# Optimization experiments

Hardware: AMD Instinct MI355X
Metric: run time of the kernel (lower is better)

The kernel has to match this reference:

```python
import jax, jax.numpy as jnp
import numpy as np

B, N, D = 8, 1024, 768
H = 12
HD = D // H


def setup_inputs() -> dict:
    key = jax.random.key(0)
    ks = jax.random.split(key, 9)
    s = 1.0 / np.sqrt(D)
    return {
        "x": jax.random.normal(ks[0], (B, N, D), dtype=jnp.float32),
        "Wq": jax.random.normal(ks[1], (D, D), dtype=jnp.float32) * s,
        "bq": jax.random.normal(ks[2], (D,), dtype=jnp.float32) * 0.02,
        "Wk": jax.random.normal(ks[3], (D, D), dtype=jnp.float32) * s,
        "bk": jax.random.normal(ks[4], (D,), dtype=jnp.float32) * 0.02,
        "Wv": jax.random.normal(ks[5], (D, D), dtype=jnp.float32) * s,
        "bv": jax.random.normal(ks[6], (D,), dtype=jnp.float32) * 0.02,
        "Wo": jax.random.normal(ks[7], (D, D), dtype=jnp.float32) * s,
        "bo": jax.random.normal(ks[8], (D,), dtype=jnp.float32) * 0.02,
    }


def _softmax_one(x):
    # quiet softmax: exp(x - max) / (1 + sum exp(x - max))
    x = x - jnp.max(x, axis=-1, keepdims=True)
    ex = jnp.exp(x)
    return ex / (1.0 + jnp.sum(ex, axis=-1, keepdims=True))


def reference(x, Wq, bq, Wk, bk, Wv, bv, Wo, bo):
    q = x @ Wq + bq  # [B,N,D]
    k = x @ Wk + bk
    v = x @ Wv + bv
    # split heads -> [B,H,N,HD]
    qs = q.reshape(B, N, H, HD).transpose(0, 2, 1, 3)
    ks = k.reshape(B, N, H, HD).transpose(0, 2, 1, 3)
    vs = v.reshape(B, N, H, HD).transpose(0, 2, 1, 3)
    scores = jnp.einsum("bhqd,bhkd->bhqk", qs, ks) / np.sqrt(HD)
    attn = _softmax_one(scores)  # quiet_attention=True
    ctx = jnp.einsum("bhqk,bhkd->bhqd", attn, vs)
    ctx = ctx.transpose(0, 2, 1, 3).reshape(B, N, D)
    return ctx @ Wo + bo
```

## Files before the change

kernel.cpp:

```cpp
#include <hip/hip_runtime.h>
#include <cstdint>

#define DEV __device__ __forceinline__

typedef __bf16 bf16x4 __attribute__((ext_vector_type(4)));
typedef __bf16 bf16x8 __attribute__((ext_vector_type(8)));
typedef float  floatx4 __attribute__((ext_vector_type(4)));
typedef short  short4v __attribute__((ext_vector_type(4)));

constexpr int BB = 8, NSEQ = 1024, DMODEL = 768, NH = 12, HD = 64;
constexpr int MTOK = BB * NSEQ;
constexpr int NQKV = 3 * DMODEL;
constexpr float CS = 0.18033688011112042f;

DEV void async_copy16(void* lds, const void* g) {
    __builtin_amdgcn_global_load_lds(
        (__attribute__((address_space(1))) void*)(const_cast<void*>(g)),
        (__attribute__((address_space(3))) void*)lds,
        16, 0, 0);
}

DEV floatx4 mfma16x32(bf16x8 a, bf16x8 b, floatx4 c) {
    return __builtin_amdgcn_mfma_f32_16x16x32_bf16(a, b, c, 0, 0, 0);
}
DEV floatx4 mfma16x16(bf16x4 a, bf16x4 b, floatx4 c) {
    return __builtin_amdgcn_mfma_f32_16x16x16bf16_1k(
        __builtin_bit_cast(short4v, a), __builtin_bit_cast(short4v, b), c, 0, 0, 0);
}


__global__ __launch_bounds__(256) void k_prep(const float* __restrict__ x,
                                              __bf16* __restrict__ xb,
                                              const float* __restrict__ Wq,
                                              const float* __restrict__ Wk,
                                              const float* __restrict__ Wv,
                                              const float* __restrict__ Wo,
                                              __bf16* __restrict__ wtqkv,
                                              __bf16* __restrict__ wto,
                                              const float* __restrict__ bq,
                                              const float* __restrict__ bk,
                                              const float* __restrict__ bv,
                                              float* __restrict__ bqkv) {
    __shared__ float tile[32][33];
    int bid = blockIdx.x, t = threadIdx.x;
    if (bid < 6144) {
        int i = (bid * 256 + t) * 4;
        float4 v = *(const float4*)(x + i);
        bf16x4 o;
        o[0] = (__bf16)v.x; o[1] = (__bf16)v.y; o[2] = (__bf16)v.z; o[3] = (__bf16)v.w;
        *(bf16x4*)(xb + i) = o;
    } else if (bid < 8448) {
        int idx = bid - 6144;
        int z = idx / 576, rem = idx % 576;
        int k0 = (rem % 24) * 32, n0 = (rem / 24) * 32;
        const float* W = (z == 0) ? Wq : (z == 1) ? Wk : (z == 2) ? Wv : Wo;
        int tx = t & 31, ty = t >> 5;
#pragma unroll
        for (int p = 0; p < 4; p++)
            tile[ty + 8 * p][tx] = W[(size_t)(k0 + ty + 8 * p) * 768 + n0 + tx];
        __syncthreads();
        __bf16* out = (z < 3) ? (wtqkv + (size_t)z * 768 * 768) : wto;
#pragma unroll
        for (int p = 0; p < 4; p++)
            out[(size_t)(n0 + ty + 8 * p) * 768 + k0 + tx] = (__bf16)tile[tx][ty + 8 * p];
    } else {
        int i = (bid - 8448) * 256 + t;
        if (i < 768) bqkv[i] = bq[i];
        else if (i < 1536) bqkv[i] = bk[i - 768];
        else bqkv[i] = bv[i - 1536];
    }
}

template <typename OutT, bool QKV, int BN>
__global__ __launch_bounds__(256) void k_gemm(const __bf16* __restrict__ A,
                                              const __bf16* __restrict__ Bt,
                                              const float* __restrict__ bias,
                                              OutT* __restrict__ C, int Nn,
                                              __bf16* __restrict__ qfb,
                                              __bf16* __restrict__ kfb,
                                              __bf16* __restrict__ vfb) {
    constexpr int CT = BN / 32;
    constexpr int NBI = BN / 32;
    __shared__ __align__(16) __bf16 As[128 * 64];
    __shared__ __align__(16) __bf16 Bs[BN * 64];
    int t = threadIdx.x, lane = t & 63, w = t >> 6;
    int quad = lane >> 4, n16 = lane & 15;
    int wm = w & 1, wn = w >> 1;
    int m0 = blockIdx.x * 128, n0 = blockIdx.y * BN;
    floatx4 acc[4][CT] = {};

    for (int k0 = 0; k0 < 768; k0 += 64) {
        __syncthreads();
#pragma unroll
        for (int i = 0; i < 4; i++) {
            int off = t + i * 256;
            int row = off >> 3, pc = off & 7;
            int c = pc ^ (row & 7);
            async_copy16(&As[row * 64 + pc * 8],
                         &A[(size_t)(m0 + row) * 768 + k0 + c * 8]);
        }
#pragma unroll
        for (int i = 0; i < NBI; i++) {
            int off = t + i * 256;
            int row = off >> 3, pc = off & 7;
            int c = pc ^ (row & 7);
            async_copy16(&Bs[row * 64 + pc * 8],
                         &Bt[(size_t)(n0 + row) * 768 + k0 + c * 8]);
        }
        __builtin_amdgcn_s_waitcnt(0);
        __syncthreads();
#pragma unroll
        for (int kfi = 0; kfi < 2; kfi++) {
            bf16x8 a[4], bfr[CT];
#pragma unroll
            for (int rt = 0; rt < 4; rt++) {
                int row = wm * 64 + rt * 16 + n16;
                a[rt] = *(const bf16x8*)&As[row * 64 + ((quad + 4 * kfi) ^ (row & 7)) * 8];
            }
#pragma unroll
            for (int ct = 0; ct < CT; ct++) {
                int row = wn * (BN / 2) + ct * 16 + n16;
                bfr[ct] = *(const bf16x8*)&Bs[row * 64 + ((quad + 4 * kfi) ^ (row & 7)) * 8];
            }
#pragma unroll
            for (int rt = 0; rt < 4; rt++)
#pragma unroll
                for (int ct = 0; ct < CT; ct++)
                    acc[rt][ct] = mfma16x32(a[rt], bfr[ct], acc[rt][ct]);
        }
    }

    if (QKV) {
        if (n0 >= 1536) {
#pragma unroll
            for (int ct = 0; ct < CT; ct++) {
                int col = n0 + wn * (BN / 2) + ct * 16 + n16;
                float bs = bias[col];
                int cz = col - 1536;
                int hh = cz >> 6, hd = cz & 63;
                int mg = hd >> 4, l16 = hd & 15;
#pragma unroll
                for (int rt = 0; rt < 4; rt++) {
                    int row0 = m0 + wm * 64 + rt * 16 + quad * 4;
                    int bb = row0 >> 10, key = row0 & 1023;
                    int kt = key >> 6, wv = (key >> 4) & 3, qd = (key >> 2) & 3;
                    bf16x4 pk;
#pragma unroll
                    for (int r = 0; r < 4; r++) pk[r] = (__bf16)(acc[rt][ct][r] + bs);
                    size_t idx = ((((size_t)(bb * 12 + hh) * 16 + kt) * 4 + wv) * 4 + mg) * 256
                                 + (size_t)(qd * 16 + l16) * 4;
                    *(bf16x4*)&vfb[idx] = pk;
                }
            }
        } else {
            __bf16* dst = (n0 < 768) ? qfb : kfb;
            float mult = (n0 < 768) ? CS : 1.0f;
            int cofs = (n0 < 768) ? 0 : 768;
#pragma unroll
            for (int ct = 0; ct < CT; ct++) {
                int col = n0 + wn * (BN / 2) + ct * 16 + n16;
                float bs = bias[col];
                int cz = col - cofs;
                int hh = cz >> 6, hd = cz & 63;
                int kfi = hd >> 5, qd2 = (hd >> 3) & 3, j = hd & 7;
#pragma unroll
                for (int rt = 0; rt < 4; rt++) {
                    int row0 = m0 + wm * 64 + rt * 16 + quad * 4;
                    int bb = row0 >> 10, q = row0 & 1023;
                    int t16 = q >> 4, nn = q & 15;
                    size_t idx = (((size_t)(bb * 12 + hh) * 64 + t16) * 2 + kfi) * 512
                                 + (size_t)(qd2 * 16 + nn) * 8 + j;
#pragma unroll
                    for (int r = 0; r < 4; r++)
                        dst[idx + (size_t)r * 8] = (__bf16)((acc[rt][ct][r] + bs) * mult);
                }
            }
        }
    } else {
#pragma unroll
        for (int ct = 0; ct < CT; ct++) {
            int col = n0 + wn * (BN / 2) + ct * 16 + n16;
            float bs = bias[col];
#pragma unroll
            for (int rt = 0; rt < 4; rt++) {
#pragma unroll
                for (int r = 0; r < 4; r++) {
                    int row = m0 + wm * 64 + rt * 16 + quad * 4 + r;
                    C[(size_t)row * Nn + col] = (OutT)(acc[rt][ct][r] + bs);
                }
            }
        }
    }
}

__global__ __launch_bounds__(256) void k_attn(const __bf16* __restrict__ QF,
                                              const __bf16* __restrict__ KF,
                                              const __bf16* __restrict__ VF,
                                              __bf16* __restrict__ ctx) {
    __shared__ __align__(16) unsigned char smem[18432];
    float* buf0 = (float*)smem;
    float* buf1 = (float*)(smem + 8704);
    float* Lsum = (float*)(smem + 17408);
    float* Pmax = (float*)(smem + 17920);

    int t = threadIdx.x, lane = t & 63, w = t >> 6;
    int quad = lane >> 4, n16 = lane & 15;
    int id = blockIdx.x;
    int bB = id & 7;
    int seq = id >> 3;
    int h = seq % 12;
    int qt = seq / 12;
    int q0 = qt * 32;
    int bh = bB * NH + h;

    bf16x8 qf[2][2];
    {
        const __bf16* qp = QF + (size_t)(bh * 64 + qt * 2) * 1024 + lane * 8;
#pragma unroll
        for (int ng = 0; ng < 2; ng++)
#pragma unroll
            for (int kfi = 0; kfi < 2; kfi++)
                qf[ng][kfi] = *(const bf16x8*)(qp + (ng * 2 + kfi) * 512);
    }
    const __bf16* kp = KF + (size_t)(bh * 64 + w) * 1024 + lane * 8;
    const __bf16* vp = VF + ((size_t)bh * 16 * 4 + w) * 1024 + lane * 4;

    floatx4 acc[4][2] = {};
    float rs[2] = {0.f, 0.f};
    float pm[2] = {0.f, 0.f};

    auto compute = [&](bf16x8 (&kf)[2], bf16x4 (&vf)[4]) {
        floatx4 s[2] = {};
#pragma unroll
        for (int ng = 0; ng < 2; ng++)
#pragma unroll
            for (int kfi = 0; kfi < 2; kfi++)
                s[ng] = mfma16x32(kf[kfi], qf[ng][kfi], s[ng]);
        bf16x4 pb[2];
#pragma unroll
        for (int ng = 0; ng < 2; ng++) {
#pragma unroll
            for (int r = 0; r < 4; r++) {
                float p = __builtin_amdgcn_exp2f(s[ng][r]);
                rs[ng] += p;
                pm[ng] = fmaxf(pm[ng], p);
                pb[ng][r] = (__bf16)p;
            }
        }
#pragma unroll
        for (int mg = 0; mg < 4; mg++)
#pragma unroll
            for (int ng = 0; ng < 2; ng++)
                acc[mg][ng] = mfma16x16(vf[mg], pb[ng], acc[mg][ng]);
    };

    bf16x8 kf0[2], kf1[2];
    bf16x4 vf0[4], vf1[4];
    kf0[0] = *(const bf16x8*)kp;
    kf0[1] = *(const bf16x8*)(kp + 512);
#pragma unroll
    for (int mg = 0; mg < 4; mg++) vf0[mg] = *(const bf16x4*)(vp + mg * 256);
    kp += 4096; vp += 4096;

    for (int kt = 0; kt < 16; kt += 2) {
        kf1[0] = *(const bf16x8*)kp;
        kf1[1] = *(const bf16x8*)(kp + 512);
#pragma unroll
        for (int mg = 0; mg < 4; mg++) vf1[mg] = *(const bf16x4*)(vp + mg * 256);
        kp += 4096; vp += 4096;
        compute(kf0, vf0);
        if (kt < 14) {
            kf0[0] = *(const bf16x8*)kp;
            kf0[1] = *(const bf16x8*)(kp + 512);
#pragma unroll
            for (int mg = 0; mg < 4; mg++) vf0[mg] = *(const bf16x4*)(vp + mg * 256);
            kp += 4096; vp += 4096;
        }
        compute(kf1, vf1);
    }

#pragma unroll
    for (int ng = 0; ng < 2; ng++) {
        rs[ng] += __shfl_xor(rs[ng], 16);
        rs[ng] += __shfl_xor(rs[ng], 32);
        pm[ng] = fmaxf(pm[ng], __shfl_xor(pm[ng], 16));
        pm[ng] = fmaxf(pm[ng], __shfl_xor(pm[ng], 32));
    }
    if (quad < 2) {
        Lsum[w * 32 + quad * 16 + n16] = quad ? rs[1] : rs[0];
        Pmax[w * 32 + quad * 16 + n16] = quad ? pm[1] : pm[0];
    }
    __syncthreads();

    float* mybuf = (w & 1) ? buf1 : buf0;
    if (w < 2) {
#pragma unroll
        for (int mg = 0; mg < 4; mg++)
#pragma unroll
            for (int ng = 0; ng < 2; ng++)
                *(floatx4*)&mybuf[(ng * 16 + n16) * 68 + mg * 16 + quad * 4] = acc[mg][ng];
    }
    __syncthreads();
    if (w >= 2) {
#pragma unroll
        for (int mg = 0; mg < 4; mg++)
#pragma unroll
            for (int ng = 0; ng < 2; ng++) {
                float* p = &mybuf[(ng * 16 + n16) * 68 + mg * 16 + quad * 4];
                floatx4 cur = *(const floatx4*)p;
                *(floatx4*)p = cur + acc[mg][ng];
            }
    }
    __syncthreads();

    int qrow = t >> 3;
    int hh = (t & 7) * 8;
    float l = Lsum[qrow] + Lsum[32 + qrow] + Lsum[64 + qrow] + Lsum[96 + qrow];
    float pmx = fmaxf(fmaxf(Pmax[qrow], Pmax[32 + qrow]),
                      fmaxf(Pmax[64 + qrow], Pmax[96 + qrow]));
    float invd = 1.f / (pmx + l);
    floatx4 v0 = *(const floatx4*)&buf0[qrow * 68 + hh];
    floatx4 v1 = *(const floatx4*)&buf0[qrow * 68 + hh + 4];
    floatx4 u0 = *(const floatx4*)&buf1[qrow * 68 + hh];
    floatx4 u1 = *(const floatx4*)&buf1[qrow * 68 + hh + 4];
    bf16x8 o;
#pragma unroll
    for (int j = 0; j < 4; j++) o[j] = (__bf16)((v0[j] + u0[j]) * invd);
#pragma unroll
    for (int j = 0; j < 4; j++) o[j + 4] = (__bf16)((v1[j] + u1[j]) * invd);
    __bf16* dst = ctx + (size_t)(bB * NSEQ + q0 + qrow) * DMODEL + h * 64 + hh;
    *(bf16x8*)dst = o;
}

extern "C" void kernel_launch(void* const* d_in, const int* in_sizes, int n_in,
                              void* d_out, int out_size, void* d_ws, size_t ws_size,
                              hipStream_t stream) {
    (void)in_sizes; (void)n_in; (void)out_size;
    const float* x  = (const float*)d_in[0];
    const float* Wq = (const float*)d_in[1];
    const float* bq = (const float*)d_in[2];
    const float* Wk = (const float*)d_in[3];
    const float* bk = (const float*)d_in[4];
    const float* Wv = (const float*)d_in[5];
    const float* bv = (const float*)d_in[6];
    const float* Wo = (const float*)d_in[7];
    const float* bo = (const float*)d_in[8];
    float* out = (float*)d_out;

    char* ws = (char*)d_ws;
    size_t off = 0;
    auto alloc = [&](size_t bytes) {
        void* p = ws + off;
        off += (bytes + 255) & ~(size_t)255;
        return p;
    };
    __bf16* xb    = (__bf16*)alloc((size_t)MTOK * DMODEL * 2);
    __bf16* wtqkv = (__bf16*)alloc((size_t)NQKV * DMODEL * 2);
    __bf16* wto   = (__bf16*)alloc((size_t)DMODEL * DMODEL * 2);
    float*  bqkv  = (float*)alloc((size_t)NQKV * 4);
    __bf16* qfb   = (__bf16*)alloc((size_t)MTOK * DMODEL * 2);
    __bf16* kfb   = (__bf16*)alloc((size_t)MTOK * DMODEL * 2);
    __bf16* vfb   = (__bf16*)alloc((size_t)MTOK * DMODEL * 2);
    if (off > ws_size) return;
    __bf16* ctx = xb;

    k_prep<<<dim3(8457), dim3(256), 0, stream>>>(x, xb, Wq, Wk, Wv, Wo, wtqkv, wto,
                                                 bq, bk, bv, bqkv);
    k_gemm<__bf16, true, 128><<<dim3(64, 18), dim3(256), 0, stream>>>(
        xb, wtqkv, bqkv, (__bf16*)nullptr, NQKV, qfb, kfb, vfb);
    k_attn<<<dim3(3072), dim3(256), 0, stream>>>(qfb, kfb, vfb, ctx);
    k_gemm<float, false, 64><<<dim3(64, 12), dim3(256), 0, stream>>>(
        ctx, wto, bo, out, DMODEL, nullptr, nullptr, nullptr);
}
```

Baseline: 207.8 us.

## Add dedicated 256x128 QKV GEMM kernel with triple-buffered async LDS pipeline

Replaces the generic QKV projection GEMM launch with a dedicated kernel that uses 512 threads and a 256x128 tile. It triple-buffers A/B tiles in LDS via async global-to-LDS copies, overlapping prefetch of tile kt+2 with MFMA work on tile kt using vmcnt-based waits. MFMA sections also run at raised wave priority. The goal is to hide global memory latency and raise reuse per block, at the cost of 144KB of LDS per block (one block per CU) and fewer blocks (576).

Result: no change. 205.9 us (-0.9%).

```diff
diff --git a/kernel.cpp b/kernel.cpp
--- a/kernel.cpp
+++ b/kernel.cpp
@@ -71,6 +71,136 @@
     }
 }
 
+__global__ __launch_bounds__(512) void k_qkv(const __bf16* __restrict__ A,
+                                             const __bf16* __restrict__ Bt,
+                                             const float* __restrict__ bias,
+                                             __bf16* __restrict__ qfb,
+                                             __bf16* __restrict__ kfb,
+                                             __bf16* __restrict__ vfb) {
+    constexpr int SLOT = 24576;
+    __shared__ __align__(16) __bf16 lds[3 * SLOT];
+    int t = threadIdx.x, lane = t & 63, w = t >> 6;
+    int quad = lane >> 4, n16 = lane & 15;
+    int wm = w >> 1, wn = w & 1;
+    int m0 = blockIdx.x * 256, n0 = blockIdx.y * 128;
+    floatx4 acc[4][4] = {};
+
+    auto stage_part = [&](__bf16* slot, int k0, int p) {
+        __bf16* As_ = slot;
+        __bf16* Bs_ = slot + 16384;
+#pragma unroll
+        for (int i = 2 * p; i < 2 * p + 2; i++) {
+            int off = t + i * 512;
+            int row = off >> 3, pc = off & 7;
+            int c = pc ^ (row & 7);
+            async_copy16(&As_[row * 64 + pc * 8],
+                         &A[(size_t)(m0 + row) * 768 + k0 + c * 8]);
+        }
+        {
+            int off = t + p * 512;
+            int row = off >> 3, pc = off & 7;
+            int c = pc ^ (row & 7);
+            async_copy16(&Bs_[row * 64 + pc * 8],
+                         &Bt[(size_t)(n0 + row) * 768 + k0 + c * 8]);
+        }
+    };
+
+    stage_part(lds, 0, 0);
+    stage_part(lds, 0, 1);
+    stage_part(lds + SLOT, 64, 0);
+    stage_part(lds + SLOT, 64, 1);
+    asm volatile("s_waitcnt vmcnt(6)\n\ts_barrier" ::: "memory");
+    __builtin_amdgcn_sched_barrier(0);
+
+#pragma unroll
+    for (int kt = 0; kt < 12; kt++) {
+        __bf16* As_ = lds + (kt % 3) * SLOT;
+        __bf16* Bs_ = As_ + 16384;
+        __bf16* pf = lds + ((kt + 2) % 3) * SLOT;
+        int pk0 = (kt + 2) * 64;
+        bool do_pf = (kt + 2 < 12);
+
+#pragma unroll
+        for (int kfi = 0; kfi < 2; kfi++) {
+            if (do_pf) stage_part(pf, pk0, kfi);
+            bf16x8 a[4], bfr[4];
+#pragma unroll
+            for (int rt = 0; rt < 4; rt++) {
+                int row = wm * 64 + rt * 16 + n16;
+                a[rt] = *(const bf16x8*)&As_[row * 64 + ((quad + 4 * kfi) ^ (row & 7)) * 8];
+            }
+#pragma unroll
+            for (int ct = 0; ct < 4; ct++) {
+                int row = wn * 64 + ct * 16 + n16;
+                bfr[ct] = *(const bf16x8*)&Bs_[row * 64 + ((quad + 4 * kfi) ^ (row & 7)) * 8];
+            }
+            __builtin_amdgcn_s_setprio(1);
+#pragma unroll
+            for (int rt = 0; rt < 4; rt++)
+#pragma unroll
+                for (int ct = 0; ct < 4; ct++)
+                    acc[rt][ct] = mfma16x32(a[rt], bfr[ct], acc[rt][ct]);
+            __builtin_amdgcn_s_setprio(0);
+        }
+
+        if (kt < 11) {
+            __builtin_amdgcn_sched_barrier(0);
+            if (kt < 10) {
+                asm volatile("s_waitcnt vmcnt(6)\n\ts_barrier" ::: "memory");
+            } else {
+                asm volatile("s_waitcnt vmcnt(0)\n\ts_barrier" ::: "memory");
+            }
+            __builtin_amdgcn_sched_barrier(0);
+        }
+    }
+
+    if (n0 >= 1536) {
+#pragma unroll
+        for (int ct = 0; ct < 4; ct++) {
+            int col = n0 + wn * 64 + ct * 16 + n16;
+            float bs = bias[col];
+            int cz = col - 1536;
+            int hh = cz >> 6, hd = cz & 63;
+            int mg = hd >> 4, l16 = hd & 15;
+#pragma unroll
+            for (int rt = 0; rt < 4; rt++) {
+                int row0 = m0 + wm * 64 + rt * 16 + quad * 4;
+                int bb = row0 >> 10, key = row0 & 1023;
+                int ktv = key >> 6, wv = (key >> 4) & 3, qd = (key >> 2) & 3;
+                bf16x4 pk;
+#pragma unroll
+                for (int r = 0; r < 4; r++) pk[r] = (__bf16)(acc[rt][ct][r] + bs);
+                size_t idx = ((((size_t)(bb * 12 + hh) * 16 + ktv) * 4 + wv) * 4 + mg) * 256
+                             + (size_t)(qd * 16 + l16) * 4;
+                *(bf16x4*)&vfb[idx] = pk;
+            }
+        }
+    } else {
+        __bf16* dst = (n0 < 768) ? qfb : kfb;
+        float mult = (n0 < 768) ? CS : 1.0f;
+        int cofs = (n0 < 768) ? 0 : 768;
+#pragma unroll
+        for (int ct = 0; ct < 4; ct++) {
+            int col = n0 + wn * 64 + ct * 16 + n16;
+            float bs = bias[col];
+            int cz = col - cofs;
+            int hh = cz >> 6, hd = cz & 63;
+            int kfi = hd >> 5, qd2 = (hd >> 3) & 3, j = hd & 7;
+#pragma unroll
+            for (int rt = 0; rt < 4; rt++) {
+                int row0 = m0 + wm * 64 + rt * 16 + quad * 4;
+                int bb = row0 >> 10, q = row0 & 1023;
+                int t16 = q >> 4, nn = q & 15;
+                size_t idx = (((size_t)(bb * 12 + hh) * 64 + t16) * 2 + kfi) * 512
+                             + (size_t)(qd2 * 16 + nn) * 8 + j;
+#pragma unroll
+                for (int r = 0; r < 4; r++)
+                    dst[idx + (size_t)r * 8] = (__bf16)((acc[rt][ct][r] + bs) * mult);
+            }
+        }
+    }
+}
+
 template <typename OutT, bool QKV, int BN>
 __global__ __launch_bounds__(256) void k_gemm(const __bf16* __restrict__ A,
                                               const __bf16* __restrict__ Bt,
@@ -131,51 +261,6 @@
     }
 
     if (QKV) {
-        if (n0 >= 1536) {
-#pragma unroll
-            for (int ct = 0; ct < CT; ct++) {
-                int col = n0 + wn * (BN / 2) + ct * 16 + n16;
-                float bs = bias[col];
-                int cz = col - 1536;
-                int hh = cz >> 6, hd = cz & 63;
-                int mg = hd >> 4, l16 = hd & 15;
-#pragma unroll
-                for (int rt = 0; rt < 4; rt++) {
-                    int row0 = m0 + wm * 64 + rt * 16 + quad * 4;
-                    int bb = row0 >> 10, key = row0 & 1023;
-                    int kt = key >> 6, wv = (key >> 4) & 3, qd = (key >> 2) & 3;
-                    bf16x4 pk;
-#pragma unroll
-                    for (int r = 0; r < 4; r++) pk[r] = (__bf16)(acc[rt][ct][r] + bs);
-                    size_t idx = ((((size_t)(bb * 12 + hh) * 16 + kt) * 4 + wv) * 4 + mg) * 256
-                                 + (size_t)(qd * 16 + l16) * 4;
-                    *(bf16x4*)&vfb[idx] = pk;
-                }
-            }
-        } else {
-            __bf16* dst = (n0 < 768) ? qfb : kfb;
-            float mult = (n0 < 768) ? CS : 1.0f;
-            int cofs = (n0 < 768) ? 0 : 768;
-#pragma unroll
-            for (int ct = 0; ct < CT; ct++) {
-                int col = n0 + wn * (BN / 2) + ct * 16 + n16;
-                float bs = bias[col];
-                int cz = col - cofs;
-                int hh = cz >> 6, hd = cz & 63;
-                int kfi = hd >> 5, qd2 = (hd >> 3) & 3, j = hd & 7;
-#pragma unroll
-                for (int rt = 0; rt < 4; rt++) {
-                    int row0 = m0 + wm * 64 + rt * 16 + quad * 4;
-                    int bb = row0 >> 10, q = row0 & 1023;
-                    int t16 = q >> 4, nn = q & 15;
-                    size_t idx = (((size_t)(bb * 12 + hh) * 64 + t16) * 2 + kfi) * 512
-                                 + (size_t)(qd2 * 16 + nn) * 8 + j;
-#pragma unroll
-                    for (int r = 0; r < 4; r++)
-                        dst[idx + (size_t)r * 8] = (__bf16)((acc[rt][ct][r] + bs) * mult);
-                }
-            }
-        }
     } else {
 #pragma unroll
         for (int ct = 0; ct < CT; ct++) {
@@ -366,8 +451,7 @@
 
     k_prep<<<dim3(8457), dim3(256), 0, stream>>>(x, xb, Wq, Wk, Wv, Wo, wtqkv, wto,
                                                  bq, bk, bv, bqkv);
-    k_gemm<__bf16, true, 128><<<dim3(64, 18), dim3(256), 0, stream>>>(
-        xb, wtqkv, bqkv, (__bf16*)nullptr, NQKV, qfb, kfb, vfb);
+    k_qkv<<<dim3(32, 18), dim3(512), 0, stream>>>(xb, wtqkv, bqkv, qfb, kfb, vfb);
     k_attn<<<dim3(3072), dim3(256), 0, stream>>>(qfb, kfb, vfb, ctx);
     k_gemm<float, false, 64><<<dim3(64, 12), dim3(256), 0, stream>>>(
         ctx, wto, bo, out, DMODEL, nullptr, nullptr, nullptr);
```
